# Optimization experiments

Measured on AMD Instinct MI355X. Metric: run time of the kernel, lower is better.

The kernel has to match this reference:

```python
import jax, jax.numpy as jnp
import numpy as np

HEADS, DIM, SEQ_LEN, MEM_LEN, CMEM_LEN, CMEM_RATIO = 16, 1024, 512, 512, 128, 4
DIM_H = DIM // HEADS


def shift(x):
    # relative-position shift trick, same as torch version
    *lead, i, j = x.shape
    x = jnp.concatenate([x, jnp.zeros((*lead, i, i), x.dtype)], -1)
    l = i + j - 1
    x = x.reshape(*lead, -1)
    pad = (-x.shape[-1]) % l
    x = jnp.concatenate([x, jnp.zeros((*lead, pad), x.dtype)], -1)
    x = x.reshape(*lead, -1, l)
    return x[..., :i, i - 1:]


def merge_heads(t):
    b, n, _ = t.shape
    return t.reshape(b, n, HEADS, DIM_H).transpose(0, 2, 1, 3)  # [b,h,n,dh]


def conv_compress(mem, conv_w, conv_b):
    # Conv1d(dim, dim, k=ratio, stride=ratio) == blockwise einsum
    b, L, e = mem.shape
    blocks = mem.reshape(b, L // CMEM_RATIO, CMEM_RATIO, e)
    return jnp.einsum('bmri,oir->bmo', blocks, conv_w) + conv_b


def full_attn(q, k, v):
    dots = jnp.einsum('bhid,bhjd->bhij', q, k) * (q.shape[-1] ** -0.5)
    attn = jax.nn.softmax(dots, axis=-1)
    return jnp.einsum('bhij,bhjd->bhid', attn, v)


def setup_inputs() -> dict:
    key = jax.random.key(0)
    ks = jax.random.split(key, 10)
    b = 8
    kv_len = CMEM_LEN + MEM_LEN + SEQ_LEN
    s = 0.02
    return {
        'x': jax.random.normal(ks[0], (b, SEQ_LEN, DIM), jnp.float32),
        'mem': jax.random.normal(ks[1], (b, MEM_LEN, DIM), jnp.float32),
        'cmem': jax.random.normal(ks[2], (b, CMEM_LEN, DIM), jnp.float32),
        'pos_emb': jax.random.normal(ks[3], (HEADS, kv_len, DIM_H), jnp.float32),
        'Wq': jax.random.normal(ks[4], (DIM, DIM), jnp.float32) * s,
        'Wkv': jax.random.normal(ks[5], (DIM, 2 * DIM), jnp.float32) * s,
        'Wout': jax.random.normal(ks[6], (DIM, DIM), jnp.float32) * s,
        'bout': jnp.zeros((DIM,), jnp.float32),
        'conv_w': jax.random.normal(ks[7], (DIM, DIM, CMEM_RATIO), jnp.float32) * s,
        'conv_b': jnp.zeros((DIM,), jnp.float32),
    }


def reference(x, mem, cmem, pos_emb, Wq, Wkv, Wout, bout, conv_w, conv_b):
    b, t, e = x.shape
    scale = DIM_H ** -0.5
    mem_len, cmem_len = mem.shape[1], cmem.shape[1]

    q = x @ Wq
    kv_input = jnp.concatenate([cmem, mem, x], axis=1)
    kv_len = kv_input.shape[1]
    k, v = jnp.split(kv_input @ Wkv, 2, axis=-1)
    q, k, v = map(merge_heads, (q, k, v))  # [b,h,n,dh]

    dots = jnp.einsum('bhid,bhjd->bhij', q, k) * scale
    pe = pos_emb[:, -kv_len:].astype(q.dtype)
    pos_dots = shift(jnp.einsum('bhid,hjd->bhij', q, pe) * scale)
    dots = dots + pos_dots

    attn = jax.nn.softmax(dots, axis=-1)
    weights = attn
    out = jnp.einsum('bhij,bhjd->bhid', attn, v)
    out = out.transpose(0, 2, 1, 3).reshape(b, t, -1)
    logits = out @ Wout + bout

    # memory update (queue_fifo with length mem_len)
    queue = jnp.concatenate([mem, x], axis=1)
    old_mem, new_mem = queue[:, :-MEM_LEN], queue[:, -MEM_LEN:]
    # old_mem length (512) divisible by cmem_ratio -> no padding branch
    compressed_mem = conv_compress(old_mem, conv_w, conv_b)
    new_cmem = jnp.concatenate([cmem, compressed_mem], axis=1)[:, -CMEM_LEN:]

    # auxiliary reconstruction loss (detached paths)
    old_mem_d = jax.lax.stop_gradient(old_mem)
    cm2 = conv_compress(old_mem_d, conv_w, conv_b)
    cmem_k, cmem_v = jnp.split(cm2 @ jax.lax.stop_gradient(Wkv), 2, axis=-1)
    cmem_k, cmem_v = map(merge_heads, (cmem_k, cmem_v))
    lo = kv_len - min(mem_len, MEM_LEN) - SEQ_LEN
    hi = kv_len - SEQ_LEN
    old_mem_k = jax.lax.stop_gradient(k[:, :, lo:hi])
    old_mem_v = jax.lax.stop_gradient(v[:, :, lo:hi])
    q_d = jax.lax.stop_gradient(q)
    aux_loss = jnp.mean((full_attn(q_d, old_mem_k, old_mem_v)
                         - full_attn(q_d, cmem_k, cmem_v)) ** 2)

    return logits, new_mem, new_cmem, aux_loss, weights
```

## Files before the change

kernel.cpp:

```cpp
#include <hip/hip_runtime.h>
#include <cstdint>


typedef __bf16 bf16;
typedef __bf16 bf16x2 __attribute__((ext_vector_type(2)));
typedef __bf16 bf16x4 __attribute__((ext_vector_type(4)));
typedef __bf16 bf16x8 __attribute__((ext_vector_type(8)));
typedef float  f32x2  __attribute__((ext_vector_type(2)));
typedef float  f32x4  __attribute__((ext_vector_type(4)));

#define GLOAD_LDS16(g, l) \
    __builtin_amdgcn_global_load_lds((const __attribute__((address_space(1))) void*)(g), \
                                     (__attribute__((address_space(3))) void*)(l), 16, 0, 0)

template<int AMODE, int EPI>
__global__ __launch_bounds__(256)
void mfma_gemm(const bf16* __restrict__ A, const bf16* __restrict__ B2,
               float* __restrict__ C, bf16* __restrict__ outB, bf16* __restrict__ vT,
               int N, int K, int lda, int ldbt, int ldc,
               const float* __restrict__ bias, int vrows,
               const bf16* __restrict__ gcmem, const bf16* __restrict__ gmem,
               const bf16* __restrict__ gx)
{
    int row0 = blockIdx.y * 128, col0 = blockIdx.x * 128;
    int tid = threadIdx.x;
    int kofs = (EPI == 8) ? blockIdx.z * K : 0;

    __shared__ bf16 As[128 * 32];
    __shared__ bf16 Bs[128 * 32];

    int lane = tid & 63, wid = tid >> 6;
    int wr = wid >> 1, wc = wid & 1;
    int fr = lane & 15, fq = lane >> 4;

    int srow = lane >> 2;
    int sc16 = (lane & 3) ^ ((lane >> 3) & 3);
    const bf16* aq[2];
    const bf16* bq[2];
    bf16* as_dst[2];
    bf16* bs_dst[2];
#pragma unroll
    for (int t = 0; t < 2; t++) {
        int gr = row0 + wid * 32 + t * 16 + srow;
        const bf16* ap;
        if (AMODE == 0) {
            ap = A + (long)gr * lda + kofs;
        } else {
            int bb = gr / 1152, rr = gr - bb * 1152;
            ap = (rr < 128) ? (gcmem + ((long)bb * 128 + rr) * 1024)
               : (rr < 640) ? (gmem + ((long)bb * 512 + (rr - 128)) * 1024)
                            : (gx   + ((long)bb * 512 + (rr - 640)) * 1024);
        }
        aq[t] = ap + sc16 * 8;
        int gc = col0 + wid * 32 + t * 16 + srow;
        bq[t] = B2 + (long)gc * ldbt + kofs + sc16 * 8;
        as_dst[t] = &As[(wid * 32 + t * 16) * 32];
        bs_dst[t] = &Bs[(wid * 32 + t * 16) * 32];
    }

    int sfq = (fq ^ ((fr >> 1) & 3)) * 8;

    f32x4 acc[4][4];
#pragma unroll
    for (int i = 0; i < 4; i++)
#pragma unroll
        for (int j = 0; j < 4; j++) acc[i][j] = (f32x4){0.f, 0.f, 0.f, 0.f};

    for (int k0 = 0; k0 < K; k0 += 32) {
#pragma unroll
        for (int t = 0; t < 2; t++) {
            GLOAD_LDS16(aq[t] + k0, as_dst[t]);
            GLOAD_LDS16(bq[t] + k0, bs_dst[t]);
        }
        __syncthreads();

        bf16x8 af[4], bfv[4];
#pragma unroll
        for (int i = 0; i < 4; i++)
            af[i] = *(const bf16x8*)&As[(wr * 64 + i * 16 + fr) * 32 + sfq];
#pragma unroll
        for (int j = 0; j < 4; j++)
            bfv[j] = *(const bf16x8*)&Bs[(wc * 64 + j * 16 + fr) * 32 + sfq];
#pragma unroll
        for (int i = 0; i < 4; i++)
#pragma unroll
            for (int j = 0; j < 4; j++)
                acc[i][j] = __builtin_amdgcn_mfma_f32_16x16x32_bf16(af[i], bfv[j], acc[i][j], 0, 0, 0);
        __syncthreads();
    }

#pragma unroll
    for (int i = 0; i < 4; i++) {
#pragma unroll
        for (int j = 0; j < 4; j++) {
#pragma unroll
            for (int g = 0; g < 4; g++) {
                int r = row0 + wr * 64 + i * 16 + fq * 4 + g;
                int c = col0 + wc * 64 + j * 16 + fr;
                float v = acc[i][j][g];
                if (EPI == 0) {
                    if (bias) v += bias[c];
                    C[(long)r * ldc + c] = v;
                } else if (EPI == 6) {
                    if (bias) v += bias[c];
                    __builtin_nontemporal_store(v, &C[(long)r * ldc + c]);
                } else if (EPI == 8) {
                    C[((long)blockIdx.z << 20) + (long)r * 1024 + c] = v;
                } else if (EPI == 4) {
                    outB[(long)r * ldc + c] = (bf16)v;
                } else {
                    if (c < 1024) {
                        outB[(long)r * 1024 + c] = (bf16)v;
                    } else {
                        int d = c - 1024; int hh = d >> 6; d &= 63;
                        int bb = r / vrows; int j2 = r - bb * vrows;
                        vT[(((long)(bb * 16 + hh)) * 64 + d) * vrows + j2] = (bf16)v;
                    }
                }
            }
        }
    }
}

__global__ __launch_bounds__(256)
void splitk_reduce(const float* __restrict__ pbuf, const float* __restrict__ bias,
                   float* __restrict__ outF, bf16* __restrict__ outB)
{
    int i = blockIdx.x * 256 + threadIdx.x;
    f32x4 s = reinterpret_cast<const f32x4*>(pbuf)[i];
#pragma unroll
    for (int k = 1; k < 4; k++) {
        f32x4 t = reinterpret_cast<const f32x4*>(pbuf + (long)k * 1048576)[i];
        s[0] += t[0]; s[1] += t[1]; s[2] += t[2]; s[3] += t[3];
    }
    int col4 = (i << 2) & 1023;
    f32x4 bv = *(const f32x4*)&bias[col4];
    s[0] += bv[0]; s[1] += bv[1]; s[2] += bv[2]; s[3] += bv[3];
    reinterpret_cast<f32x4*>(outF)[i] = s;
    bf16x4 h = { (bf16)s[0], (bf16)s[1], (bf16)s[2], (bf16)s[3] };
    reinterpret_cast<bf16x4*>(outB)[i] = h;
}

__global__ __launch_bounds__(256)
void transpose_cast(const float* __restrict__ in, bf16* __restrict__ out, int R, int C)
{
    __shared__ float t[32][33];
    int c0 = blockIdx.x * 32, r0 = blockIdx.y * 32;
    int tx = threadIdx.x & 31, ty = threadIdx.x >> 5;
#pragma unroll
    for (int i = 0; i < 32; i += 8)
        t[ty + i][tx] = in[(long)(r0 + ty + i) * C + c0 + tx];
    __syncthreads();
#pragma unroll
    for (int i = 0; i < 32; i += 8)
        out[(long)(c0 + ty + i) * R + r0 + tx] = (bf16)t[tx][ty + i];
}

__global__ __launch_bounds__(256)
void convw_cast(const float* __restrict__ cw, bf16* __restrict__ out)
{
    long o = blockIdx.x;
    const float* src = cw + o * 4096;
    bf16* dst = out + o * 4096;
    __shared__ float t[4096];
#pragma unroll
    for (int k = 0; k < 4; k++)
        *(f32x4*)&t[(threadIdx.x + k * 256) * 4] = *(const f32x4*)&src[(threadIdx.x + k * 256) * 4];
    __syncthreads();
#pragma unroll
    for (int k = 0; k < 8; k++) {
        int d2 = 2 * (threadIdx.x + k * 256);
        int pi = ((d2 & 1023) << 2) | (d2 >> 10);
        bf16x2 h = { (bf16)t[pi], (bf16)t[pi + 4] };
        *(bf16x2*)&dst[d2] = h;
    }
}

__global__ __launch_bounds__(256)
void cast_f2b_multi(const float* __restrict__ s0, bf16* __restrict__ d0, int n0,
                    const float* __restrict__ s1, bf16* __restrict__ d1, int n1,
                    const float* __restrict__ s2, bf16* __restrict__ d2, int n2,
                    const float* __restrict__ s3, bf16* __restrict__ d3, int n3,
                    float* __restrict__ xmirror)
{
    int i = blockIdx.x * 256 + threadIdx.x;
    int stride = gridDim.x * 256;
    int ntot = n0 + n1 + n2 + n3;
    for (; i < ntot; i += stride) {
        const float* src; bf16* dst; int k = i; int seg;
        if (k < n0) { src = s0; dst = d0; seg = 0; }
        else if ((k -= n0) < n1) { src = s1; dst = d1; seg = 1; }
        else if ((k -= n1) < n2) { src = s2; dst = d2; seg = 2; }
        else { k -= n2; src = s3; dst = d3; seg = 3; }
        f32x4 f = reinterpret_cast<const f32x4*>(src)[k];
        bf16x4 h = { (bf16)f[0], (bf16)f[1], (bf16)f[2], (bf16)f[3] };
        reinterpret_cast<bf16x4*>(dst)[k] = h;
        if (seg == 1)
            __builtin_nontemporal_store(f, &reinterpret_cast<f32x4*>(xmirror)[k]);
    }
}

#define SSTR 1164

__global__ __launch_bounds__(256)
void attn_fused16(const bf16* __restrict__ qb, const bf16* __restrict__ kb,
                  const bf16* __restrict__ peb, const bf16* __restrict__ vTb,
                  float* __restrict__ weights, bf16* __restrict__ oatb)
{
    int bid = blockIdx.x;
    int w = (bid & 7) * 512 + (bid >> 3);
    int z = w >> 5;
    int b = z >> 4, h = z & 15;
    int r0 = (w & 31) * 16;
    int tid = threadIdx.x;
    int lane = tid & 63, wid = tid >> 6;
    int fr = lane & 15, fq = lane >> 4;

    __shared__ bf16 S[16 * SSTR];

    bf16x8 afr[2];
#pragma unroll
    for (int ks = 0; ks < 2; ks++)
        afr[ks] = *(const bf16x8*)&qb[((long)(b * 512 + r0 + fr)) * 1024 + h * 64 + ks * 32 + fq * 8];

#pragma unroll 3
    for (int ch = 0; ch < 9; ch++) {
        int c0 = ch * 128;
        int jb0 = c0 + 496 - r0 + 32 * wid;

        f32x4 p[3];
#pragma unroll
        for (int ct = 0; ct < 3; ct++) {
            f32x4 a = (f32x4){0.f, 0.f, 0.f, 0.f};
            int j = jb0 + ct * 16 + fr;
            bool ok = (j < 1152);
#pragma unroll
            for (int ks = 0; ks < 2; ks++) {
                bf16x8 bv = {};
                if (ok) bv = *(const bf16x8*)&peb[((long)(h * 1152 + j)) * 64 + ks * 32 + fq * 8];
                a = __builtin_amdgcn_mfma_f32_16x16x32_bf16(afr[ks], bv, a, 0, 0, 0);
            }
            p[ct] = a;
        }

#pragma unroll
        for (int tt = 0; tt < 2; tt++) {
            int cc = 32 * wid + 16 * tt + fr;
            f32x4 a = (f32x4){0.f, 0.f, 0.f, 0.f};
            long krow = (long)(b * 1152 + c0 + cc);
#pragma unroll
            for (int ks = 0; ks < 2; ks++) {
                bf16x8 bv = *(const bf16x8*)&kb[krow * 1024 + h * 64 + ks * 32 + fq * 8];
                a = __builtin_amdgcn_mfma_f32_16x16x32_bf16(afr[ks], bv, a, 0, 0, 0);
            }
#pragma unroll
            for (int g = 0; g < 4; g++) {
                int rr = fq * 4 + g;
                int uu = fr + 15 - rr;
                int src = (uu & 15) | (fq << 4);
                float s0 = __shfl(p[tt][g], src, 64);
                float s1 = __shfl(p[tt + 1][g], src, 64);
                float pv = (uu < 16) ? s0 : s1;
                S[rr * SSTR + c0 + cc] = (bf16)(0.125f * (a[g] + pv));
            }
        }
    }
    __syncthreads();

    for (int rw = 0; rw < 4; rw++) {
        int row = wid * 4 + rw;
        bf16* Srow = &S[row * SSTR];
        bf16x8 v0 = *(const bf16x8*)&Srow[lane * 8];
        bf16x8 v1 = *(const bf16x8*)&Srow[512 + lane * 8];
        bf16x2 v2 = *(const bf16x2*)&Srow[1024 + lane * 2];
        float e[18];
#pragma unroll
        for (int j = 0; j < 8; j++) { e[j] = (float)v0[j]; e[8 + j] = (float)v1[j]; }
        e[16] = (float)v2[0]; e[17] = (float)v2[1];

        float m = e[0];
#pragma unroll
        for (int k = 1; k < 18; k++) m = fmaxf(m, e[k]);
#pragma unroll
        for (int off = 32; off; off >>= 1) m = fmaxf(m, __shfl_xor(m, off, 64));
        float sm = 0.f;
#pragma unroll
        for (int k = 0; k < 18; k++) { e[k] = __expf(e[k] - m); sm += e[k]; }
#pragma unroll
        for (int off = 32; off; off >>= 1) sm += __shfl_xor(sm, off, 64);
        float inv = 1.f / sm;

        bf16x8 w0, w1; bf16x2 w2;
#pragma unroll
        for (int j = 0; j < 8; j++) { w0[j] = (bf16)(e[j] * inv); w1[j] = (bf16)(e[8 + j] * inv); }
        w2[0] = (bf16)(e[16] * inv); w2[1] = (bf16)(e[17] * inv);
        *(bf16x8*)&Srow[lane * 8] = w0;
        *(bf16x8*)&Srow[512 + lane * 8] = w1;
        *(bf16x2*)&Srow[1024 + lane * 2] = w2;
    }
    __syncthreads();

    f32x4 oacc = (f32x4){0.f, 0.f, 0.f, 0.f};
    int dt = wid;
    for (int ch = 0; ch < 9; ch++) {
        int c0 = ch * 128;
#pragma unroll
        for (int ks = 0; ks < 4; ks++) {
            bf16x8 pa = *(const bf16x8*)&S[fr * SSTR + c0 + ks * 32 + fq * 8];
            bf16x8 vb = *(const bf16x8*)&vTb[((long)z * 64 + dt * 16 + fr) * 1152 + c0 + ks * 32 + fq * 8];
            oacc = __builtin_amdgcn_mfma_f32_16x16x32_bf16(pa, vb, oacc, 0, 0, 0);
        }
    }
#pragma unroll
    for (int g = 0; g < 4; g++)
        oatb[((long)(b * 512 + r0 + fq * 4 + g)) * 1024 + h * 64 + dt * 16 + fr] = (bf16)oacc[g];

    for (int rw = 0; rw < 4; rw++) {
        int row = wid * 4 + rw;
        const bf16* Srow = &S[row * SSTR];
        long wbase = ((long)z * 512 + r0 + row) * 1152;
        bf16x8 v0 = *(const bf16x8*)&Srow[lane * 8];
        bf16x8 v1 = *(const bf16x8*)&Srow[512 + lane * 8];
        bf16x2 v2 = *(const bf16x2*)&Srow[1024 + lane * 2];
        f32x4 a0 = { (float)v0[0], (float)v0[1], (float)v0[2], (float)v0[3] };
        f32x4 a1 = { (float)v0[4], (float)v0[5], (float)v0[6], (float)v0[7] };
        f32x4 b0 = { (float)v1[0], (float)v1[1], (float)v1[2], (float)v1[3] };
        f32x4 b1 = { (float)v1[4], (float)v1[5], (float)v1[6], (float)v1[7] };
        f32x2 c0 = { (float)v2[0], (float)v2[1] };
        __builtin_nontemporal_store(a0, (f32x4*)&weights[wbase + lane * 8]);
        __builtin_nontemporal_store(a1, (f32x4*)&weights[wbase + lane * 8 + 4]);
        __builtin_nontemporal_store(b0, (f32x4*)&weights[wbase + 512 + lane * 8]);
        __builtin_nontemporal_store(b1, (f32x4*)&weights[wbase + 512 + lane * 8 + 4]);
        __builtin_nontemporal_store(c0, (f32x2*)&weights[wbase + 1024 + lane * 2]);
    }
}

__global__ __launch_bounds__(256)
void aux_mfma_kernel(const bf16* __restrict__ qb, const bf16* __restrict__ kb,
                     const bf16* __restrict__ ckb,
                     const bf16* __restrict__ vTb, const bf16* __restrict__ cvT,
                     float* __restrict__ partials)
{
    int z = blockIdx.y;
    int b = z >> 4, h = z & 15;
    int r0 = blockIdx.x * 128;
    int tid = threadIdx.x;
    int lane = tid & 63, wid = tid >> 6;
    int fr = lane & 15, fq = lane >> 4;

    __shared__ bf16 qs[128][72];
    __shared__ bf16 upool[128 * 136];
    __shared__ bf16 vt[64][136];
    __shared__ float wred[4];

#pragma unroll
    for (int t = 0; t < 4; t++) {
        int e = tid + 256 * t; int rr = e >> 3, c8 = (e & 7) * 8;
        *(bf16x8*)&qs[rr][c8] = *(const bf16x8*)&qb[((long)(b * 512 + r0 + rr)) * 1024 + h * 64 + c8];
    }

    float o1[2][4][4];
    f32x4 oaccv[2][4];
    float mrow[2][4], lrow[2][4];
    f32x4 sacc[2][8];
    float local = 0.f;

    for (int pass = 0; pass < 2; pass++) {
#pragma unroll
        for (int i = 0; i < 2; i++)
#pragma unroll
            for (int g = 0; g < 4; g++) { mrow[i][g] = -3.4e38f; lrow[i][g] = 0.f; }
#pragma unroll
        for (int i = 0; i < 2; i++)
#pragma unroll
            for (int jd = 0; jd < 4; jd++) oaccv[i][jd] = (f32x4){0.f, 0.f, 0.f, 0.f};

        int nchunk = pass ? 1 : 4;
        for (int jt = 0; jt < nchunk; jt++) {
            __syncthreads();
            if (pass == 0) {
                long base = (long)(b * 1152 + 128 + jt * 128);
#pragma unroll
                for (int t = 0; t < 4; t++) {
                    int e = tid + 256 * t; int j = e >> 3, c8 = (e & 7) * 8;
                    *(bf16x8*)&upool[j * 72 + c8] = *(const bf16x8*)&kb[(base + j) * 1024 + h * 64 + c8];
                }
#pragma unroll
                for (int t = 0; t < 4; t++) {
                    int e = tid + 256 * t; int d = e >> 4, j8 = (e & 15) * 8;
                    *(bf16x8*)&vt[d][j8] =
                        *(const bf16x8*)&vTb[((long)z * 64 + d) * 1152 + 128 + jt * 128 + j8];
                }
            } else {
#pragma unroll
                for (int t = 0; t < 4; t++) {
                    int e = tid + 256 * t; int j = e >> 3, c8 = (e & 7) * 8;
                    *(bf16x8*)&upool[j * 72 + c8] = *(const bf16x8*)&ckb[((long)(b * 128 + j)) * 1024 + h * 64 + c8];
                }
#pragma unroll
                for (int t = 0; t < 4; t++) {
                    int e = tid + 256 * t; int d = e >> 4, j8 = (e & 15) * 8;
                    *(bf16x8*)&vt[d][j8] = *(const bf16x8*)&cvT[((long)z * 64 + d) * 128 + j8];
                }
            }
            __syncthreads();

#pragma unroll
            for (int i = 0; i < 2; i++)
#pragma unroll
                for (int j = 0; j < 8; j++) sacc[i][j] = (f32x4){0.f, 0.f, 0.f, 0.f};
#pragma unroll
            for (int s = 0; s < 2; s++) {
                bf16x8 af[2], bfv[8];
#pragma unroll
                for (int i = 0; i < 2; i++)
                    af[i] = *(const bf16x8*)&qs[wid * 32 + i * 16 + fr][s * 32 + fq * 8];
#pragma unroll
                for (int j = 0; j < 8; j++)
                    bfv[j] = *(const bf16x8*)&upool[(j * 16 + fr) * 72 + s * 32 + fq * 8];
#pragma unroll
                for (int i = 0; i < 2; i++)
#pragma unroll
                    for (int j = 0; j < 8; j++)
                        sacc[i][j] = __builtin_amdgcn_mfma_f32_16x16x32_bf16(af[i], bfv[j], sacc[i][j], 0, 0, 0);
            }
            __syncthreads();

#pragma unroll
            for (int i = 0; i < 2; i++) {
#pragma unroll
                for (int g = 0; g < 4; g++) {
                    float mx = -3.4e38f;
#pragma unroll
                    for (int j = 0; j < 8; j++) mx = fmaxf(mx, sacc[i][j][g]);
                    mx *= 0.125f;
#pragma unroll
                    for (int msk = 1; msk <= 8; msk <<= 1) mx = fmaxf(mx, __shfl_xor(mx, msk, 64));
                    float mnew = fmaxf(mrow[i][g], mx);
                    float alpha = __expf(mrow[i][g] - mnew);
                    mrow[i][g] = mnew;
                    float sum = 0.f;
                    int prow = (wid * 32 + i * 16 + fq * 4 + g) * 136;
#pragma unroll
                    for (int j = 0; j < 8; j++) {
                        float p = __expf(sacc[i][j][g] * 0.125f - mnew);
                        sum += p;
                        upool[prow + j * 16 + fr] = (bf16)p;
                    }
#pragma unroll
                    for (int msk = 1; msk <= 8; msk <<= 1) sum += __shfl_xor(sum, msk, 16);
                    lrow[i][g] = lrow[i][g] * alpha + sum;
#pragma unroll
                    for (int jd = 0; jd < 4; jd++) oaccv[i][jd][g] *= alpha;
                }
            }
            __syncthreads();

#pragma unroll
            for (int s2 = 0; s2 < 4; s2++) {
                bf16x8 pa[2], vb[4];
#pragma unroll
                for (int i = 0; i < 2; i++)
                    pa[i] = *(const bf16x8*)&upool[(wid * 32 + i * 16 + fr) * 136 + s2 * 32 + fq * 8];
#pragma unroll
                for (int jd = 0; jd < 4; jd++)
                    vb[jd] = *(const bf16x8*)&vt[jd * 16 + fr][s2 * 32 + fq * 8];
#pragma unroll
                for (int i = 0; i < 2; i++)
#pragma unroll
                    for (int jd = 0; jd < 4; jd++)
                        oaccv[i][jd] = __builtin_amdgcn_mfma_f32_16x16x32_bf16(pa[i], vb[jd], oaccv[i][jd], 0, 0, 0);
            }
        }

        if (pass == 0) {
#pragma unroll
            for (int i = 0; i < 2; i++)
#pragma unroll
                for (int jd = 0; jd < 4; jd++)
#pragma unroll
                    for (int g = 0; g < 4; g++)
                        o1[i][jd][g] = oaccv[i][jd][g] / lrow[i][g];
        } else {
#pragma unroll
            for (int i = 0; i < 2; i++)
#pragma unroll
                for (int jd = 0; jd < 4; jd++)
#pragma unroll
                    for (int g = 0; g < 4; g++) {
                        float dd = o1[i][jd][g] - oaccv[i][jd][g] / lrow[i][g];
                        local += dd * dd;
                    }
        }
    }

#pragma unroll
    for (int off = 32; off; off >>= 1) local += __shfl_xor(local, off, 64);
    if (lane == 0) wred[wid] = local;
    __syncthreads();
    if (tid == 0)
        partials[(long)blockIdx.y * 4 + blockIdx.x] = wred[0] + wred[1] + wred[2] + wred[3];
}

__global__ __launch_bounds__(256)
void aux_reduce_kernel(const float* __restrict__ partials, float* __restrict__ out)
{
    int tid = threadIdx.x;
    __shared__ float wred[4];
    float s = 0.f;
    for (int i = tid; i < 512; i += 256) s += partials[i];
#pragma unroll
    for (int off = 32; off; off >>= 1) s += __shfl_xor(s, off, 64);
    if ((tid & 63) == 0) wred[tid >> 6] = s;
    __syncthreads();
    if (tid == 0) out[0] = (wred[0] + wred[1] + wred[2] + wred[3]) * (1.0f / 4194304.0f);
}

extern "C" void kernel_launch(void* const* d_in, const int* in_sizes, int n_in,
                              void* d_out, int out_size, void* d_ws, size_t ws_size,
                              hipStream_t stream)
{
    const float* x      = (const float*)d_in[0];
    const float* mem    = (const float*)d_in[1];
    const float* cmem   = (const float*)d_in[2];
    const float* pe     = (const float*)d_in[3];
    const float* Wq     = (const float*)d_in[4];
    const float* Wkv    = (const float*)d_in[5];
    const float* Wout   = (const float*)d_in[6];
    const float* bout   = (const float*)d_in[7];
    const float* conv_w = (const float*)d_in[8];
    const float* conv_b = (const float*)d_in[9];

    float* out_logits  = (float*)d_out;
    float* out_newmem  = out_logits + 4194304;
    float* out_newcmem = out_newmem + 4194304;
    float* out_aux     = out_newcmem + 1048576;
    float* out_weights = out_aux + 1;

    float* ws       = (float*)d_ws;
    float* partials = ws;
    float* pbuf     = partials + 4096;
    bf16* bws     = (bf16*)(pbuf + 4194304);
    bf16* WqTb    = bws;
    bf16* WkvTb   = WqTb + 1048576;
    bf16* WoutTb  = WkvTb + 2097152;
    bf16* convwTb = WoutTb + 1048576;
    bf16* vTb     = convwTb + 4194304;
    bf16* cvT     = vTb + 9437184;
    bf16* qb      = cvT + 1048576;
    bf16* kb      = qb + 4194304;
    bf16* ckb     = kb + 9437184;
    bf16* peb     = ckb + 1048576;
    bf16* xb      = peb + 1179648;
    bf16* memb    = xb + 4194304;
    bf16* cmemb   = memb + 4194304;
    bf16* ncmemb  = cmemb + 1048576;
    bf16* oatb    = ncmemb + 1048576;

    dim3 blk(256);

    transpose_cast<<<dim3(32, 32), blk, 0, stream>>>(Wq, WqTb, 1024, 1024);
    transpose_cast<<<dim3(64, 32), blk, 0, stream>>>(Wkv, WkvTb, 1024, 2048);
    transpose_cast<<<dim3(32, 32), blk, 0, stream>>>(Wout, WoutTb, 1024, 1024);
    convw_cast<<<dim3(1024), blk, 0, stream>>>(conv_w, convwTb);
    cast_f2b_multi<<<dim3(2048), blk, 0, stream>>>(
        pe, peb, 294912, x, xb, 1048576, mem, memb, 1048576, cmem, cmemb, 262144,
        out_newmem);

    mfma_gemm<0, 4><<<dim3(8, 32, 1), blk, 0, stream>>>(
        xb, WqTb, nullptr, qb, nullptr, 1024, 1024, 1024, 1024, 1024,
        nullptr, 0, nullptr, nullptr, nullptr);

    mfma_gemm<1, 5><<<dim3(16, 72, 1), blk, 0, stream>>>(
        nullptr, WkvTb, nullptr, kb, vTb, 2048, 1024, 1024, 1024, 2048,
        nullptr, 1152, cmemb, memb, xb);

    mfma_gemm<0, 8><<<dim3(8, 8, 4), blk, 0, stream>>>(
        memb, convwTb, pbuf, nullptr, nullptr, 1024, 1024, 4096, 4096, 1024,
        nullptr, 0, nullptr, nullptr, nullptr);
    splitk_reduce<<<dim3(1024), blk, 0, stream>>>(pbuf, conv_b, out_newcmem, ncmemb);

    mfma_gemm<0, 5><<<dim3(16, 8, 1), blk, 0, stream>>>(
        ncmemb, WkvTb, nullptr, ckb, cvT, 2048, 1024, 1024, 1024, 2048,
        nullptr, 128, nullptr, nullptr, nullptr);

    attn_fused16<<<dim3(4096), blk, 0, stream>>>(qb, kb, peb, vTb, out_weights, oatb);

    mfma_gemm<0, 6><<<dim3(8, 32, 1), blk, 0, stream>>>(
        oatb, WoutTb, out_logits, nullptr, nullptr, 1024, 1024, 1024, 1024, 1024,
        bout, 0, nullptr, nullptr, nullptr);

    aux_mfma_kernel<<<dim3(4, 128), blk, 0, stream>>>(qb, kb, ckb, vTb, cvT, partials);
    aux_reduce_kernel<<<dim3(1), blk, 0, stream>>>(partials, out_aux);
}
```

Before: 533.8 us.

## Merge independent GEMM and attention launches into grouped multi-role kernels

Turns the GEMM, attention and aux kernels into device-function bodies and dispatches them by block index inside three combined kernels: Q/KV/conv GEMMs together, compressed-KV GEMM with attention, and output projection with the aux loss. This cuts launch count and lets independent work fill the GPU concurrently instead of running serially with tail gaps. In exchange, shared memory is sized to the largest role, which can lower occupancy for the smaller roles, and register use becomes the maximum across roles.

```diff
diff --git a/kernel.cpp b/kernel.cpp
--- a/kernel.cpp
+++ b/kernel.cpp
@@ -14,20 +14,19 @@
                                      (__attribute__((address_space(3))) void*)(l), 16, 0, 0)
 
 template<int AMODE, int EPI>
-__global__ __launch_bounds__(256)
-void mfma_gemm(const bf16* __restrict__ A, const bf16* __restrict__ B2,
-               float* __restrict__ C, bf16* __restrict__ outB, bf16* __restrict__ vT,
-               int N, int K, int lda, int ldbt, int ldc,
-               const float* __restrict__ bias, int vrows,
-               const bf16* __restrict__ gcmem, const bf16* __restrict__ gmem,
-               const bf16* __restrict__ gx)
-{
-    int row0 = blockIdx.y * 128, col0 = blockIdx.x * 128;
+__device__ __forceinline__ void gemm_body(
+    int bx, int by, int bz,
+    const bf16* __restrict__ A, const bf16* __restrict__ B2,
+    float* __restrict__ C, bf16* __restrict__ outB, bf16* __restrict__ vT,
+    int N, int K, int lda, int ldbt, int ldc,
+    const float* __restrict__ bias, int vrows,
+    const bf16* __restrict__ gcmem, const bf16* __restrict__ gmem,
+    const bf16* __restrict__ gx,
+    bf16* As, bf16* Bs)
+{
+    int row0 = by * 128, col0 = bx * 128;
     int tid = threadIdx.x;
-    int kofs = (EPI == 8) ? blockIdx.z * K : 0;
-
-    __shared__ bf16 As[128 * 32];
-    __shared__ bf16 Bs[128 * 32];
+    int kofs = (EPI == 8) ? bz * K : 0;
 
     int lane = tid & 63, wid = tid >> 6;
     int wr = wid >> 1, wc = wid & 1;
@@ -105,7 +104,7 @@
                     if (bias) v += bias[c];
                     __builtin_nontemporal_store(v, &C[(long)r * ldc + c]);
                 } else if (EPI == 8) {
-                    C[((long)blockIdx.z << 20) + (long)r * 1024 + c] = v;
+                    C[((long)bz << 20) + (long)r * 1024 + c] = v;
                 } else if (EPI == 4) {
                     outB[(long)r * ldc + c] = (bf16)v;
                 } else {
@@ -122,92 +121,13 @@
     }
 }
 
-__global__ __launch_bounds__(256)
-void splitk_reduce(const float* __restrict__ pbuf, const float* __restrict__ bias,
-                   float* __restrict__ outF, bf16* __restrict__ outB)
-{
-    int i = blockIdx.x * 256 + threadIdx.x;
-    f32x4 s = reinterpret_cast<const f32x4*>(pbuf)[i];
-#pragma unroll
-    for (int k = 1; k < 4; k++) {
-        f32x4 t = reinterpret_cast<const f32x4*>(pbuf + (long)k * 1048576)[i];
-        s[0] += t[0]; s[1] += t[1]; s[2] += t[2]; s[3] += t[3];
-    }
-    int col4 = (i << 2) & 1023;
-    f32x4 bv = *(const f32x4*)&bias[col4];
-    s[0] += bv[0]; s[1] += bv[1]; s[2] += bv[2]; s[3] += bv[3];
-    reinterpret_cast<f32x4*>(outF)[i] = s;
-    bf16x4 h = { (bf16)s[0], (bf16)s[1], (bf16)s[2], (bf16)s[3] };
-    reinterpret_cast<bf16x4*>(outB)[i] = h;
-}
-
-__global__ __launch_bounds__(256)
-void transpose_cast(const float* __restrict__ in, bf16* __restrict__ out, int R, int C)
-{
-    __shared__ float t[32][33];
-    int c0 = blockIdx.x * 32, r0 = blockIdx.y * 32;
-    int tx = threadIdx.x & 31, ty = threadIdx.x >> 5;
-#pragma unroll
-    for (int i = 0; i < 32; i += 8)
-        t[ty + i][tx] = in[(long)(r0 + ty + i) * C + c0 + tx];
-    __syncthreads();
-#pragma unroll
-    for (int i = 0; i < 32; i += 8)
-        out[(long)(c0 + ty + i) * R + r0 + tx] = (bf16)t[tx][ty + i];
-}
-
-__global__ __launch_bounds__(256)
-void convw_cast(const float* __restrict__ cw, bf16* __restrict__ out)
-{
-    long o = blockIdx.x;
-    const float* src = cw + o * 4096;
-    bf16* dst = out + o * 4096;
-    __shared__ float t[4096];
-#pragma unroll
-    for (int k = 0; k < 4; k++)
-        *(f32x4*)&t[(threadIdx.x + k * 256) * 4] = *(const f32x4*)&src[(threadIdx.x + k * 256) * 4];
-    __syncthreads();
-#pragma unroll
-    for (int k = 0; k < 8; k++) {
-        int d2 = 2 * (threadIdx.x + k * 256);
-        int pi = ((d2 & 1023) << 2) | (d2 >> 10);
-        bf16x2 h = { (bf16)t[pi], (bf16)t[pi + 4] };
-        *(bf16x2*)&dst[d2] = h;
-    }
-}
-
-__global__ __launch_bounds__(256)
-void cast_f2b_multi(const float* __restrict__ s0, bf16* __restrict__ d0, int n0,
-                    const float* __restrict__ s1, bf16* __restrict__ d1, int n1,
-                    const float* __restrict__ s2, bf16* __restrict__ d2, int n2,
-                    const float* __restrict__ s3, bf16* __restrict__ d3, int n3,
-                    float* __restrict__ xmirror)
-{
-    int i = blockIdx.x * 256 + threadIdx.x;
-    int stride = gridDim.x * 256;
-    int ntot = n0 + n1 + n2 + n3;
-    for (; i < ntot; i += stride) {
-        const float* src; bf16* dst; int k = i; int seg;
-        if (k < n0) { src = s0; dst = d0; seg = 0; }
-        else if ((k -= n0) < n1) { src = s1; dst = d1; seg = 1; }
-        else if ((k -= n1) < n2) { src = s2; dst = d2; seg = 2; }
-        else { k -= n2; src = s3; dst = d3; seg = 3; }
-        f32x4 f = reinterpret_cast<const f32x4*>(src)[k];
-        bf16x4 h = { (bf16)f[0], (bf16)f[1], (bf16)f[2], (bf16)f[3] };
-        reinterpret_cast<bf16x4*>(dst)[k] = h;
-        if (seg == 1)
-            __builtin_nontemporal_store(f, &reinterpret_cast<f32x4*>(xmirror)[k]);
-    }
-}
-
 #define SSTR 1164
 
-__global__ __launch_bounds__(256)
-void attn_fused16(const bf16* __restrict__ qb, const bf16* __restrict__ kb,
-                  const bf16* __restrict__ peb, const bf16* __restrict__ vTb,
-                  float* __restrict__ weights, bf16* __restrict__ oatb)
-{
-    int bid = blockIdx.x;
+__device__ __forceinline__ void attn_body(
+    int bid, const bf16* __restrict__ qb, const bf16* __restrict__ kb,
+    const bf16* __restrict__ peb, const bf16* __restrict__ vTb,
+    float* __restrict__ weights, bf16* __restrict__ oatb, bf16* S)
+{
     int w = (bid & 7) * 512 + (bid >> 3);
     int z = w >> 5;
     int b = z >> 4, h = z & 15;
@@ -215,8 +135,6 @@
     int tid = threadIdx.x;
     int lane = tid & 63, wid = tid >> 6;
     int fr = lane & 15, fq = lane >> 4;
-
-    __shared__ bf16 S[16 * SSTR];
 
     bf16x8 afr[2];
 #pragma unroll
@@ -335,28 +253,25 @@
     }
 }
 
-__global__ __launch_bounds__(256)
-void aux_mfma_kernel(const bf16* __restrict__ qb, const bf16* __restrict__ kb,
-                     const bf16* __restrict__ ckb,
-                     const bf16* __restrict__ vTb, const bf16* __restrict__ cvT,
-                     float* __restrict__ partials)
-{
-    int z = blockIdx.y;
+__device__ __forceinline__ void aux_body(
+    int bx, int by,
+    const bf16* __restrict__ qb, const bf16* __restrict__ kb,
+    const bf16* __restrict__ ckb,
+    const bf16* __restrict__ vTb, const bf16* __restrict__ cvT,
+    float* __restrict__ partials,
+    bf16* qs, bf16* upool, bf16* vt, float* wred)
+{
+    int z = by;
     int b = z >> 4, h = z & 15;
-    int r0 = blockIdx.x * 128;
+    int r0 = bx * 128;
     int tid = threadIdx.x;
     int lane = tid & 63, wid = tid >> 6;
     int fr = lane & 15, fq = lane >> 4;
 
-    __shared__ bf16 qs[128][72];
-    __shared__ bf16 upool[128 * 136];
-    __shared__ bf16 vt[64][136];
-    __shared__ float wred[4];
-
 #pragma unroll
     for (int t = 0; t < 4; t++) {
         int e = tid + 256 * t; int rr = e >> 3, c8 = (e & 7) * 8;
-        *(bf16x8*)&qs[rr][c8] = *(const bf16x8*)&qb[((long)(b * 512 + r0 + rr)) * 1024 + h * 64 + c8];
+        *(bf16x8*)&qs[rr * 72 + c8] = *(const bf16x8*)&qb[((long)(b * 512 + r0 + rr)) * 1024 + h * 64 + c8];
     }
 
     float o1[2][4][4];
@@ -388,7 +303,7 @@
 #pragma unroll
                 for (int t = 0; t < 4; t++) {
                     int e = tid + 256 * t; int d = e >> 4, j8 = (e & 15) * 8;
-                    *(bf16x8*)&vt[d][j8] =
+                    *(bf16x8*)&vt[d * 136 + j8] =
                         *(const bf16x8*)&vTb[((long)z * 64 + d) * 1152 + 128 + jt * 128 + j8];
                 }
             } else {
@@ -400,7 +315,7 @@
 #pragma unroll
                 for (int t = 0; t < 4; t++) {
                     int e = tid + 256 * t; int d = e >> 4, j8 = (e & 15) * 8;
-                    *(bf16x8*)&vt[d][j8] = *(const bf16x8*)&cvT[((long)z * 64 + d) * 128 + j8];
+                    *(bf16x8*)&vt[d * 136 + j8] = *(const bf16x8*)&cvT[((long)z * 64 + d) * 128 + j8];
                 }
             }
             __syncthreads();
@@ -414,7 +329,7 @@
                 bf16x8 af[2], bfv[8];
 #pragma unroll
                 for (int i = 0; i < 2; i++)
-                    af[i] = *(const bf16x8*)&qs[wid * 32 + i * 16 + fr][s * 32 + fq * 8];
+                    af[i] = *(const bf16x8*)&qs[(wid * 32 + i * 16 + fr) * 72 + s * 32 + fq * 8];
 #pragma unroll
                 for (int j = 0; j < 8; j++)
                     bfv[j] = *(const bf16x8*)&upool[(j * 16 + fr) * 72 + s * 32 + fq * 8];
@@ -464,7 +379,7 @@
                     pa[i] = *(const bf16x8*)&upool[(wid * 32 + i * 16 + fr) * 136 + s2 * 32 + fq * 8];
 #pragma unroll
                 for (int jd = 0; jd < 4; jd++)
-                    vb[jd] = *(const bf16x8*)&vt[jd * 16 + fr][s2 * 32 + fq * 8];
+                    vb[jd] = *(const bf16x8*)&vt[(jd * 16 + fr) * 136 + s2 * 32 + fq * 8];
 #pragma unroll
                 for (int i = 0; i < 2; i++)
 #pragma unroll
@@ -499,7 +414,153 @@
     if (lane == 0) wred[wid] = local;
     __syncthreads();
     if (tid == 0)
-        partials[(long)blockIdx.y * 4 + blockIdx.x] = wred[0] + wred[1] + wred[2] + wred[3];
+        partials[(long)by * 4 + bx] = wred[0] + wred[1] + wred[2] + wred[3];
+}
+
+__global__ __launch_bounds__(256)
+void gemmA_kernel(const bf16* __restrict__ xb, const bf16* __restrict__ memb,
+                  const bf16* __restrict__ cmemb,
+                  const bf16* __restrict__ WqTb, const bf16* __restrict__ WkvTb,
+                  const bf16* __restrict__ convwTb,
+                  bf16* __restrict__ qb, bf16* __restrict__ kb, bf16* __restrict__ vTb,
+                  float* __restrict__ pbuf)
+{
+    __shared__ bf16 As[128 * 32];
+    __shared__ bf16 Bs[128 * 32];
+    int gid = blockIdx.x;
+    if (gid < 1152) {
+        gemm_body<1, 5>(gid % 16, gid / 16, 0, nullptr, WkvTb, nullptr, kb, vTb,
+                        2048, 1024, 1024, 1024, 2048, nullptr, 1152,
+                        cmemb, memb, xb, As, Bs);
+    } else if (gid < 1408) {
+        int g = gid - 1152;
+        gemm_body<0, 4>(g % 8, g / 8, 0, xb, WqTb, nullptr, qb, nullptr,
+                        1024, 1024, 1024, 1024, 1024, nullptr, 0,
+                        nullptr, nullptr, nullptr, As, Bs);
+    } else {
+        int g = gid - 1408;
+        gemm_body<0, 8>(g % 8, (g / 8) % 8, g / 64, memb, convwTb, pbuf, nullptr, nullptr,
+                        1024, 1024, 4096, 4096, 1024, nullptr, 0,
+                        nullptr, nullptr, nullptr, As, Bs);
+    }
+}
+
+__global__ __launch_bounds__(256)
+void attn_ckv_kernel(const bf16* __restrict__ qb, const bf16* __restrict__ kb,
+                     const bf16* __restrict__ peb, const bf16* __restrict__ vTb,
+                     float* __restrict__ weights, bf16* __restrict__ oatb,
+                     const bf16* __restrict__ ncmemb, const bf16* __restrict__ WkvTb,
+                     bf16* __restrict__ ckb, bf16* __restrict__ cvT)
+{
+    __shared__ bf16 pool[16 * SSTR];
+    int gid = blockIdx.x;
+    if (gid < 128) {
+        gemm_body<0, 5>(gid % 16, gid / 16, 0, ncmemb, WkvTb, nullptr, ckb, cvT,
+                        2048, 1024, 1024, 1024, 2048, nullptr, 128,
+                        nullptr, nullptr, nullptr, pool, pool + 4096);
+    } else {
+        attn_body(gid - 128, qb, kb, peb, vTb, weights, oatb, pool);
+    }
+}
+
+__global__ __launch_bounds__(256)
+void logits_aux_kernel(const bf16* __restrict__ qb, const bf16* __restrict__ kb,
+                       const bf16* __restrict__ ckb,
+                       const bf16* __restrict__ vTb, const bf16* __restrict__ cvT,
+                       float* __restrict__ partials,
+                       const bf16* __restrict__ oatb, const bf16* __restrict__ WoutTb,
+                       float* __restrict__ out_logits, const float* __restrict__ bout)
+{
+    __shared__ bf16 pool[35328];
+    __shared__ float wred[4];
+    int gid = blockIdx.x;
+    if (gid < 512) {
+        aux_body(gid % 4, gid / 4, qb, kb, ckb, vTb, cvT, partials,
+                 pool, pool + 9216, pool + 26624, wred);
+    } else {
+        int g = gid - 512;
+        gemm_body<0, 6>(g % 8, g / 8, 0, oatb, WoutTb, out_logits, nullptr, nullptr,
+                        1024, 1024, 1024, 1024, 1024, bout, 0,
+                        nullptr, nullptr, nullptr, pool, pool + 4096);
+    }
+}
+
+__global__ __launch_bounds__(256)
+void splitk_reduce(const float* __restrict__ pbuf, const float* __restrict__ bias,
+                   float* __restrict__ outF, bf16* __restrict__ outB)
+{
+    int i = blockIdx.x * 256 + threadIdx.x;
+    f32x4 s = reinterpret_cast<const f32x4*>(pbuf)[i];
+#pragma unroll
+    for (int k = 1; k < 4; k++) {
+        f32x4 t = reinterpret_cast<const f32x4*>(pbuf + (long)k * 1048576)[i];
+        s[0] += t[0]; s[1] += t[1]; s[2] += t[2]; s[3] += t[3];
+    }
+    int col4 = (i << 2) & 1023;
+    f32x4 bv = *(const f32x4*)&bias[col4];
+    s[0] += bv[0]; s[1] += bv[1]; s[2] += bv[2]; s[3] += bv[3];
+    reinterpret_cast<f32x4*>(outF)[i] = s;
+    bf16x4 h = { (bf16)s[0], (bf16)s[1], (bf16)s[2], (bf16)s[3] };
+    reinterpret_cast<bf16x4*>(outB)[i] = h;
+}
+
+__global__ __launch_bounds__(256)
+void transpose_cast(const float* __restrict__ in, bf16* __restrict__ out, int R, int C)
+{
+    __shared__ float t[32][33];
+    int c0 = blockIdx.x * 32, r0 = blockIdx.y * 32;
+    int tx = threadIdx.x & 31, ty = threadIdx.x >> 5;
+#pragma unroll
+    for (int i = 0; i < 32; i += 8)
+        t[ty + i][tx] = in[(long)(r0 + ty + i) * C + c0 + tx];
+    __syncthreads();
+#pragma unroll
+    for (int i = 0; i < 32; i += 8)
+        out[(long)(c0 + ty + i) * R + r0 + tx] = (bf16)t[tx][ty + i];
+}
+
+__global__ __launch_bounds__(256)
+void convw_cast(const float* __restrict__ cw, bf16* __restrict__ out)
+{
+    long o = blockIdx.x;
+    const float* src = cw + o * 4096;
+    bf16* dst = out + o * 4096;
+    __shared__ float t[4096];
+#pragma unroll
+    for (int k = 0; k < 4; k++)
+        *(f32x4*)&t[(threadIdx.x + k * 256) * 4] = *(const f32x4*)&src[(threadIdx.x + k * 256) * 4];
+    __syncthreads();
+#pragma unroll
+    for (int k = 0; k < 8; k++) {
+        int d2 = 2 * (threadIdx.x + k * 256);
+        int pi = ((d2 & 1023) << 2) | (d2 >> 10);
+        bf16x2 h = { (bf16)t[pi], (bf16)t[pi + 4] };
+        *(bf16x2*)&dst[d2] = h;
+    }
+}
+
+__global__ __launch_bounds__(256)
+void cast_f2b_multi(const float* __restrict__ s0, bf16* __restrict__ d0, int n0,
+                    const float* __restrict__ s1, bf16* __restrict__ d1, int n1,
+                    const float* __restrict__ s2, bf16* __restrict__ d2, int n2,
+                    const float* __restrict__ s3, bf16* __restrict__ d3, int n3,
+                    float* __restrict__ xmirror)
+{
+    int i = blockIdx.x * 256 + threadIdx.x;
+    int stride = gridDim.x * 256;
+    int ntot = n0 + n1 + n2 + n3;
+    for (; i < ntot; i += stride) {
+        const float* src; bf16* dst; int k = i; int seg;
+        if (k < n0) { src = s0; dst = d0; seg = 0; }
+        else if ((k -= n0) < n1) { src = s1; dst = d1; seg = 1; }
+        else if ((k -= n1) < n2) { src = s2; dst = d2; seg = 2; }
+        else { k -= n2; src = s3; dst = d3; seg = 3; }
+        f32x4 f = reinterpret_cast<const f32x4*>(src)[k];
+        bf16x4 h = { (bf16)f[0], (bf16)f[1], (bf16)f[2], (bf16)f[3] };
+        reinterpret_cast<bf16x4*>(dst)[k] = h;
+        if (seg == 1)
+            __builtin_nontemporal_store(f, &reinterpret_cast<f32x4*>(xmirror)[k]);
+    }
 }
 
 __global__ __launch_bounds__(256)
@@ -567,29 +628,16 @@
         pe, peb, 294912, x, xb, 1048576, mem, memb, 1048576, cmem, cmemb, 262144,
         out_newmem);
 
-    mfma_gemm<0, 4><<<dim3(8, 32, 1), blk, 0, stream>>>(
-        xb, WqTb, nullptr, qb, nullptr, 1024, 1024, 1024, 1024, 1024,
-        nullptr, 0, nullptr, nullptr, nullptr);
-
-    mfma_gemm<1, 5><<<dim3(16, 72, 1), blk, 0, stream>>>(
-        nullptr, WkvTb, nullptr, kb, vTb, 2048, 1024, 1024, 1024, 2048,
-        nullptr, 1152, cmemb, memb, xb);
-
-    mfma_gemm<0, 8><<<dim3(8, 8, 4), blk, 0, stream>>>(
-        memb, convwTb, pbuf, nullptr, nullptr, 1024, 1024, 4096, 4096, 1024,
-        nullptr, 0, nullptr, nullptr, nullptr);
+    gemmA_kernel<<<dim3(1664), blk, 0, stream>>>(
+        xb, memb, cmemb, WqTb, WkvTb, convwTb, qb, kb, vTb, pbuf);
+
     splitk_reduce<<<dim3(1024), blk, 0, stream>>>(pbuf, conv_b, out_newcmem, ncmemb);
 
-    mfma_gemm<0, 5><<<dim3(16, 8, 1), blk, 0, stream>>>(
-        ncmemb, WkvTb, nullptr, ckb, cvT, 2048, 1024, 1024, 1024, 2048,
-        nullptr, 128, nullptr, nullptr, nullptr);
-
-    attn_fused16<<<dim3(4096), blk, 0, stream>>>(qb, kb, peb, vTb, out_weights, oatb);
-
-    mfma_gemm<0, 6><<<dim3(8, 32, 1), blk, 0, stream>>>(
-        oatb, WoutTb, out_logits, nullptr, nullptr, 1024, 1024, 1024, 1024, 1024,
-        bout, 0, nullptr, nullptr, nullptr);
-
-    aux_mfma_kernel<<<dim3(4, 128), blk, 0, stream>>>(qb, kb, ckb, vTb, cvT, partials);
+    attn_ckv_kernel<<<dim3(4224), blk, 0, stream>>>(
+        qb, kb, peb, vTb, out_weights, oatb, ncmemb, WkvTb, ckb, cvT);
+
+    logits_aux_kernel<<<dim3(768), blk, 0, stream>>>(
+        qb, kb, ckb, vTb, cvT, partials, oatb, WoutTb, out_logits, bout);
+
     aux_reduce_kernel<<<dim3(1), blk, 0, stream>>>(partials, out_aux);
 }
```

New measurement: 597.9 us. +12.0%, slower.
